# Kernel optimization log

Hardware: AMD Instinct MI355X
Metric: run time of the kernel (lower is better)

Reference implementation:

```python
import jax, jax.numpy as jnp
from jax import lax
import numpy as np

B = 16384
EPS = 1e-5


def conv2d(x, w, b, pad):
    # x: [N,C,H,W], w: [O,I,kh,kw]
    y = lax.conv_general_dilated(x, w, (1, 1), [(pad, pad), (pad, pad)],
                                 dimension_numbers=("NCHW", "OIHW", "NCHW"))
    return y + b[None, :, None, None]


def maxpool2(x):
    return lax.reduce_window(x, -jnp.inf, lax.max, (1, 1, 2, 2), (1, 1, 2, 2), "VALID")


def setup_inputs() -> dict:
    key = jax.random.key(0)
    ks = jax.random.split(key, 16)
    n = jax.random.normal
    return {
        "x": n(ks[0], (B, 1, 28, 28), dtype=jnp.float32),
        "conv1_w": n(ks[1], (8, 1, 3, 3), dtype=jnp.float32) * 0.2,
        "conv1_b": n(ks[2], (8,), dtype=jnp.float32) * 0.1,
        "conv2_w": n(ks[3], (16, 8, 3, 3), dtype=jnp.float32) * 0.1,
        "conv2_b": n(ks[4], (16,), dtype=jnp.float32) * 0.1,
        "s1_w": n(ks[5], (4, 2), dtype=jnp.float32) * 0.5,
        "s1_b": n(ks[6], (4,), dtype=jnp.float32) * 0.1,
        "s2_w": n(ks[7], (2, 4), dtype=jnp.float32) * 0.5,
        "s2_b": n(ks[8], (2,), dtype=jnp.float32) * 0.1,
        "filt_w": n(ks[9], (1, 1, 2, 2), dtype=jnp.float32) * 0.5,
        "filt_b": n(ks[10], (1,), dtype=jnp.float32) * 0.1,
        "fc1_w": n(ks[11], (64, 787), dtype=jnp.float32) * 0.03,
        "fc1_b": n(ks[12], (64,), dtype=jnp.float32) * 0.1,
        "fc2_w": n(ks[13], (4, 64), dtype=jnp.float32) * 0.1,
        "fc2_b": n(ks[14], (4,), dtype=jnp.float32) * 0.1,
        "bn_g": jnp.ones((4,), dtype=jnp.float32),
        "bn_b": jnp.zeros((4,), dtype=jnp.float32),
    }


def reference(x, conv1_w, conv1_b, conv2_w, conv2_b, s1_w, s1_b, s2_w, s2_b,
              filt_w, filt_b, fc1_w, fc1_b, fc2_w, fc2_b, bn_g, bn_b):
    bsz = x.shape[0]
    # feature extractor: conv3x3 -> relu -> maxpool2 (x2)
    f = maxpool2(jax.nn.relu(conv2d(x, conv1_w, conv1_b, 1)))        # [B,8,14,14]
    f = maxpool2(jax.nn.relu(conv2d(f, conv2_w, conv2_b, 1)))        # [B,16,7,7]
    flat = f.reshape(bsz, -1)                                        # [B,784]
    # sampler on first two features
    h = jnp.tanh(flat[:, :2] @ s1_w.T + s1_b)
    sampler_out = jax.nn.softmax(h @ s2_w.T + s2_b, axis=-1)         # [B,2]
    # conv filter: 2x2 stride-1 conv + sigmoid, mean over all patches
    logits = conv2d(x, filt_w, filt_b, 0)                            # [B,1,27,27]
    conv_out = jnp.mean(jax.nn.sigmoid(logits), axis=(1, 2, 3))[:, None]  # [B,1]
    combined = jnp.concatenate([flat, sampler_out, conv_out], axis=1)  # [B,787]
    out = jax.nn.relu(combined @ fc1_w.T + fc1_b) @ fc2_w.T + fc2_b    # [B,4]
    # BatchNorm1d, training mode (batch stats, biased variance)
    mu = jnp.mean(out, axis=0)
    var = jnp.var(out, axis=0)
    return (out - mu) * lax.rsqrt(var + EPS) * bn_g + bn_b
```

## Files before the change

kernel.cpp:

```cpp
#include <hip/hip_runtime.h>
#include <hip/hip_fp16.h>
#include <math.h>

#define NBATCH 16384
#define EPSV 1e-5f

typedef short short8 __attribute__((ext_vector_type(8)));
typedef _Float16 half8_t __attribute__((ext_vector_type(8)));
typedef short short2v __attribute__((ext_vector_type(2)));
typedef float f32x4 __attribute__((ext_vector_type(4)));
union V8 { uint4 u; short8 s; };
union VH { uint4 u; half8_t h; };

__device__ __forceinline__ unsigned short f2bf(float f) {
    unsigned int x = __float_as_uint(f);
    return (unsigned short)((x + 0x7fffu + ((x >> 16) & 1u)) >> 16);
}
__device__ __forceinline__ unsigned short f2h(float f) {
    return __half_as_ushort(__float2half(f));
}
__device__ __forceinline__ __half2 u2h(unsigned int u) { return __builtin_bit_cast(__half2, u); }
__device__ __forceinline__ unsigned int h2u(__half2 h) { return __builtin_bit_cast(unsigned int, h); }

__global__ __launch_bounds__(256) void k_prep(
    const float* __restrict__ fc1w, const float* __restrict__ w2,
    const float* __restrict__ w1, const float* __restrict__ b1,
    unsigned short* __restrict__ wt, unsigned short* __restrict__ af16,
    unsigned int* __restrict__ w1h2, unsigned int* __restrict__ b1h2)
{
    int i = blockIdx.x * 256 + threadIdx.x;
    if (i < 51200) {
        int n = i / 800, k = i - n * 800;
        float v = (k < 787) ? fc1w[n * 787 + k] : 0.f;
        wt[i] = f2h(v);
    } else if (i < 52736) {
        int a = i - 51200;
        int slot = a >> 7, rem = a & 127, oc = rem >> 3, ic = rem & 7;
        float v = (slot < 9) ? w2[oc * 72 + ic * 9 + slot] : 0.f;
        af16[a] = f2h(v);
    } else if (i < 52808) {
        int k = i - 52736;
        unsigned int hb = f2h(w1[k]);
        w1h2[k] = hb | (hb << 16);
    } else if (i < 52816) {
        int k = i - 52808;
        unsigned int hb = f2h(b1[k]);
        b1h2[k] = hb | (hb << 16);
    }
}

#define SXS 15

__global__ __launch_bounds__(64, 8) void k_conv(
    const float* __restrict__ x,
    const float* __restrict__ s1w, const float* __restrict__ s1b,
    const float* __restrict__ s2w, const float* __restrict__ s2b,
    const float* __restrict__ fw, const float* __restrict__ fb,
    const float* __restrict__ b2,
    const unsigned short* __restrict__ Afg,
    const unsigned int* __restrict__ w1h2g,
    const unsigned int* __restrict__ b1h2g,
    unsigned short* __restrict__ comb)
{
    const int l = threadIdx.x;

    __shared__ unsigned int sxu[30 * SXS];
    __shared__ __align__(16) unsigned short sf1[16 * 136];

    for (int i = l; i < 30 * SXS; i += 64) sxu[i] = 0u;
    if (l < 60) {
        int R, C;
        if (l < 16)      { R = 0;      C = l; }
        else if (l < 32) { R = 15;     C = l - 16; }
        else if (l < 46) { R = l - 31; C = 0; }
        else             { R = l - 45; C = 15; }
        *reinterpret_cast<uint4*>(&sf1[R * 136 + C * 8]) = uint4{0u, 0u, 0u, 0u};
    }

    const __half2 fwh0 = __float2half2_rn(fw[0]);
    const __half2 fwh1 = __float2half2_rn(fw[1]);
    const __half2 fwh2 = __float2half2_rn(fw[2]);
    const __half2 fwh3 = __float2half2_rn(fw[3]);
    const __half2 fbh  = __float2half2_rn(fb[0]);

    const int n = l & 15, g = l >> 4;
    const int qr = n & 7;
    const int q = (qr < 7) ? qr : 6;
    const int dr = n >> 3;
    int offs[3];
    VH af[3];
    #pragma unroll
    for (int s = 0; s < 3; ++s) {
        const int slot = s * 4 + g;
        const int u = slot / 3, v = slot - 3 * (slot / 3);
        offs[s] = (slot <= 8) ? (u * 136 + v * 8) : 0;
        af[s].u = *reinterpret_cast<const uint4*>(Afg + ((slot * 16 + n) << 3));
    }
    float biasv[4];
    #pragma unroll
    for (int i = 0; i < 4; ++i) biasv[i] = b2[4 * g + i];

    int srow[7], sww[7];
    #pragma unroll
    for (int k = 0; k < 7; ++k) {
        int u0 = l + k * 64;
        srow[k] = u0 / 15;
        sww[k]  = u0 - srow[k] * 15;
    }

    const int b = blockIdx.x;
    const float* xb = x + (size_t)b * 784;
    unsigned short* crow = comb + (size_t)b * 800;

    float xlo[7], xhi[7];
    #pragma unroll
    for (int k = 0; k < 7; ++k) {
        const int u0 = l + k * 64;
        if (u0 < 420) {
            const float* base = xb + srow[k] * 28;
            xlo[k] = (sww[k] == 0)  ? 0.f : base[2 * sww[k] - 1];
            xhi[k] = (sww[k] == 14) ? 0.f : base[2 * sww[k]];
        }
    }
    #pragma unroll
    for (int k = 0; k < 7; ++k) {
        const int u0 = l + k * 64;
        if (u0 < 420)
            sxu[(srow[k] + 1) * SXS + sww[k]] = h2u(__floats2half2_rn(xlo[k], xhi[k]));
    }

    float fsum = 0.f;
    for (int u0 = l; u0 < 378; u0 += 64) {
        int r = u0 / 14, cp = u0 - (u0 / 14) * 14;
        unsigned int A1 = sxu[(r + 1) * SXS + cp], B1 = sxu[(r + 1) * SXS + cp + 1];
        unsigned int A2 = sxu[(r + 2) * SXS + cp], B2 = sxu[(r + 2) * SXS + cp + 1];
        __half2 al1 = u2h(__builtin_amdgcn_alignbit(B1, A1, 16));
        __half2 al2 = u2h(__builtin_amdgcn_alignbit(B2, A2, 16));
        __half2 acc = __hfma2(fwh0, al1,
                      __hfma2(fwh1, u2h(B1),
                      __hfma2(fwh2, al2,
                      __hfma2(fwh3, u2h(B2), fbh))));
        float2 f = __half22float2(acc);
        fsum += __frcp_rn(1.f + __expf(-f.x));
        if (cp < 13) fsum += __frcp_rn(1.f + __expf(-f.y));
    }
    #pragma unroll
    for (int off = 32; off > 0; off >>= 1)
        fsum += __shfl_xor(fsum, off, 64);

    for (int i = l; i < 196; i += 64) {
        const int p = i / 14, j = i - (i / 14) * 14;
        unsigned int A[4], B[4], M[4];
        #pragma unroll
        for (int u = 0; u < 4; ++u) {
            A[u] = sxu[(2 * p + u) * SXS + j];
            B[u] = sxu[(2 * p + u) * SXS + j + 1];
            M[u] = __builtin_amdgcn_alignbit(B[u], A[u], 16);
        }
        unsigned short outv[8];
        #pragma unroll
        for (int oc = 0; oc < 8; ++oc) {
            __half2 a0 = u2h(b1h2g[oc]), a1 = a0;
            #pragma unroll
            for (int u = 0; u < 3; ++u) {
                #pragma unroll
                for (int v = 0; v < 3; ++v) {
                    const __half2 wv = u2h(w1h2g[oc * 9 + u * 3 + v]);
                    const unsigned int p0 = (v == 0) ? A[u]     : ((v == 1) ? M[u]     : B[u]);
                    const unsigned int p1 = (v == 0) ? A[u + 1] : ((v == 1) ? M[u + 1] : B[u + 1]);
                    a0 = __hfma2(wv, u2h(p0), a0);
                    a1 = __hfma2(wv, u2h(p1), a1);
                }
            }
            short2v s0 = __builtin_bit_cast(short2v, a0);
            short2v s1 = __builtin_bit_cast(short2v, a1);
            short2v mm = __builtin_elementwise_max(s0, s1);
            short m = mm[0] > mm[1] ? mm[0] : mm[1];
            if (m < 0) m = 0;
            outv[oc] = (unsigned short)m;
        }
        *reinterpret_cast<uint4*>(&sf1[(p + 1) * 136 + (j + 1) * 8]) =
            *reinterpret_cast<const uint4*>(outv);
    }

    float f0r = 0.f, f1r = 0.f;
    for (int pp = 0; pp < 7; ++pp) {
        const int rbase = (2 * pp + dr) * 136 + (2 * q) * 8;
        f32x4 acc0 = {0.f, 0.f, 0.f, 0.f}, acc1 = {0.f, 0.f, 0.f, 0.f};
        #pragma unroll
        for (int s = 0; s < 3; ++s) {
            VH b0, b1v;
            b0.u  = *reinterpret_cast<const uint4*>(&sf1[rbase + offs[s]]);
            b1v.u = *reinterpret_cast<const uint4*>(&sf1[rbase + 8 + offs[s]]);
            acc0 = __builtin_amdgcn_mfma_f32_16x16x32_f16(af[s].h, b0.h, acc0, 0, 0, 0);
            acc1 = __builtin_amdgcn_mfma_f32_16x16x32_f16(af[s].h, b1v.h, acc1, 0, 0, 0);
        }
        #pragma unroll
        for (int i = 0; i < 4; ++i) {
            float m = fmaxf(acc0[i], acc1[i]);
            m = fmaxf(m, __shfl_xor(m, 8, 64));
            float val = fmaxf(m + biasv[i], 0.f);
            if (pp == 0 && i == 0) {
                f0r = __shfl(val, 0, 64);
                f1r = __shfl(val, 1, 64);
            }
            if (n < 7)
                crow[(4 * g + i) * 49 + pp * 7 + q] = f2h(val);
        }
    }

    if (l < 13) crow[787 + l] = 0;
    if (l == 0) {
        crow[786] = f2h(fsum * (1.f / 729.f));
        float h[4];
        #pragma unroll
        for (int k = 0; k < 4; ++k) {
            float y = fmaf(f0r, s1w[2 * k], fmaf(f1r, s1w[2 * k + 1], s1b[k]));
            float e = __expf(2.f * y);
            h[k] = (e - 1.f) * __frcp_rn(e + 1.f);
        }
        float l0 = s2b[0], l1 = s2b[1];
        #pragma unroll
        for (int k = 0; k < 4; ++k) {
            l0 = fmaf(h[k], s2w[k], l0);
            l1 = fmaf(h[k], s2w[4 + k], l1);
        }
        float mx = fmaxf(l0, l1);
        float e0 = __expf(l0 - mx), e1 = __expf(l1 - mx);
        float inv = __frcp_rn(e0 + e1);
        crow[784] = f2h(e0 * inv);
        crow[785] = f2h(e1 * inv);
    }
}

__global__ __launch_bounds__(256) void k_fc(
    const unsigned short* __restrict__ A,
    const unsigned short* __restrict__ Bw,
    const float* __restrict__ fc1b,
    const float* __restrict__ fc2w, const float* __restrict__ fc2b,
    float* __restrict__ out, float* __restrict__ part)
{
    __shared__ uint4 Asm[2][256];
    __shared__ uint4 Bsm[2][256];
    __shared__ float sh[64][68];
    __shared__ float sfc2[4][64];
    __shared__ float pacc[4][8];

    const int t = threadIdx.x;
    const int w = t >> 6, l = t & 63;
    const int blk = blockIdx.x;

    sfc2[t >> 6][t & 63] = fc2w[t];

    const int srow = t >> 2, skbp = t & 3;
    const int skbl = skbp ^ ((srow >> 1) & 3);
    const uint4* Ag = reinterpret_cast<const uint4*>(A) + ((size_t)blk * 64 + srow) * 100;
    const uint4* Bg = reinterpret_cast<const uint4*>(Bw) + (size_t)srow * 100;
    const int sidx = srow * 4 + skbp;

    const int arow = w * 16 + (l & 15);
    const int aidx = arow * 4 + ((l >> 4) ^ ((arow >> 1) & 3));
    int bidx[4];
    #pragma unroll
    for (int nf = 0; nf < 4; ++nf) {
        int nn = nf * 16 + (l & 15);
        bidx[nf] = nn * 4 + ((l >> 4) ^ ((nn >> 1) & 3));
    }

    f32x4 acc0 = {0.f, 0.f, 0.f, 0.f}, acc1 = acc0, acc2 = acc0, acc3 = acc0;

    Asm[0][sidx] = Ag[skbl];
    Bsm[0][sidx] = Bg[skbl];

    int buf = 0;
    for (int s = 0; s < 25; ++s) {
        __syncthreads();
        if (s < 24) {
            Asm[buf ^ 1][sidx] = Ag[(s + 1) * 4 + skbl];
            Bsm[buf ^ 1][sidx] = Bg[(s + 1) * 4 + skbl];
        }
        VH av; av.u = Asm[buf][aidx];
        VH b0; b0.u = Bsm[buf][bidx[0]];
        VH b1; b1.u = Bsm[buf][bidx[1]];
        VH b2; b2.u = Bsm[buf][bidx[2]];
        VH b3; b3.u = Bsm[buf][bidx[3]];
        acc0 = __builtin_amdgcn_mfma_f32_16x16x32_f16(av.h, b0.h, acc0, 0, 0, 0);
        acc1 = __builtin_amdgcn_mfma_f32_16x16x32_f16(av.h, b1.h, acc1, 0, 0, 0);
        acc2 = __builtin_amdgcn_mfma_f32_16x16x32_f16(av.h, b2.h, acc2, 0, 0, 0);
        acc3 = __builtin_amdgcn_mfma_f32_16x16x32_f16(av.h, b3.h, acc3, 0, 0, 0);
        buf ^= 1;
    }

    {
        const int c0 = l & 15, r0 = w * 16 + (l >> 4) * 4;
        float fb0 = fc1b[c0], fb1 = fc1b[16 + c0], fb2 = fc1b[32 + c0], fb3 = fc1b[48 + c0];
        #pragma unroll
        for (int r = 0; r < 4; ++r) {
            sh[r0 + r][c0]      = fmaxf(acc0[r] + fb0, 0.f);
            sh[r0 + r][16 + c0] = fmaxf(acc1[r] + fb1, 0.f);
            sh[r0 + r][32 + c0] = fmaxf(acc2[r] + fb2, 0.f);
            sh[r0 + r][48 + c0] = fmaxf(acc3[r] + fb3, 0.f);
        }
    }
    __syncthreads();

    {
        const int row = t >> 2, oo = t & 3;
        float s = fc2b[oo];
        #pragma unroll 8
        for (int o = 0; o < 64; ++o)
            s = fmaf(sh[row][o], sfc2[oo][o], s);
        out[((size_t)blk * 64 + row) * 4 + oo] = s;

        float rs = s, rq = s * s;
        #pragma unroll
        for (int off = 4; off < 64; off <<= 1) {
            rs += __shfl_xor(rs, off, 64);
            rq += __shfl_xor(rq, off, 64);
        }
        if (l < 4) pacc[w][l] = rs;
        else if (l < 8) pacc[w][l] = rq;
    }
    __syncthreads();
    if (t < 8)
        part[blk * 8 + t] = pacc[0][t] + pacc[1][t] + pacc[2][t] + pacc[3][t];
}

__global__ void k_bnfinal(const float* __restrict__ part,
                          const float* __restrict__ g, const float* __restrict__ bb,
                          float* __restrict__ ss, int nblocks)
{
    const int t = threadIdx.x;
    float s[8];
    #pragma unroll
    for (int i = 0; i < 8; ++i) s[i] = 0.f;
    for (int idx = t; idx < nblocks; idx += 64)
        #pragma unroll
        for (int i = 0; i < 8; ++i) s[i] += part[idx * 8 + i];
    #pragma unroll
    for (int i = 0; i < 8; ++i)
        #pragma unroll
        for (int off = 32; off > 0; off >>= 1)
            s[i] += __shfl_xor(s[i], off, 64);
    if (t == 0) {
        const float invB = 1.f / 16384.f;
        #pragma unroll
        for (int j = 0; j < 4; ++j) {
            float mu = s[j] * invB;
            float var = s[4 + j] * invB - mu * mu;
            float sc = g[j] * rsqrtf(var + EPSV);
            ss[j] = sc;
            ss[4 + j] = bb[j] - mu * sc;
        }
    }
}

__global__ __launch_bounds__(256) void k_bnapply(const float* __restrict__ ss,
                                                 float* __restrict__ out)
{
    const int row = blockIdx.x * 256 + threadIdx.x;
    float4 v = reinterpret_cast<float4*>(out)[row];
    v.x = fmaf(v.x, ss[0], ss[4]);
    v.y = fmaf(v.y, ss[1], ss[5]);
    v.z = fmaf(v.z, ss[2], ss[6]);
    v.w = fmaf(v.w, ss[3], ss[7]);
    reinterpret_cast<float4*>(out)[row] = v;
}

__global__ __launch_bounds__(256) void k_transpose_fb(const float* __restrict__ in,
                                                      float* __restrict__ out)
{
    int i = blockIdx.x * 256 + threadIdx.x;
    if (i < 787 * 64) {
        int k = i >> 6, o = i & 63;
        out[i] = in[o * 787 + k];
    }
}

#define SF1F(ic, r, c) sf1[(ic) * 324 + (r) * 20 + (c)]

__global__ __launch_bounds__(256) void k_fused_fb(
    const float* __restrict__ x,
    const float* __restrict__ w1, const float* __restrict__ b1,
    const float* __restrict__ w2, const float* __restrict__ b2,
    const float* __restrict__ s1w, const float* __restrict__ s1b,
    const float* __restrict__ s2w, const float* __restrict__ s2b,
    const float* __restrict__ fw, const float* __restrict__ fb,
    const float* __restrict__ wt, const float* __restrict__ fc1b,
    const float* __restrict__ fc2w, const float* __restrict__ fc2b,
    float* __restrict__ pre)
{
    const int b = blockIdx.x;
    const int t = threadIdx.x;

    __shared__ float sxA[30][20];
    __shared__ float sxB[30][20];
    __shared__ float sf1[8 * 324];
    __shared__ float scomb[788];
    __shared__ float sw1[72];
    __shared__ float sb1[8];
    __shared__ float sw2p[16 * 76];
    __shared__ float sb2[16];
    __shared__ float sh1p[4][64];
    __shared__ float sh1[64];
    __shared__ float sred[4];
    __shared__ float ssm[27];

    for (int i = t; i < 600; i += 256) { (&sxA[0][0])[i] = 0.f; (&sxB[0][0])[i] = 0.f; }
    for (int i = t; i < 8 * 324; i += 256) sf1[i] = 0.f;
    if (t < 72) sw1[t] = w1[t];
    if (t < 8) sb1[t] = b1[t];
    for (int i = t; i < 1152; i += 256) {
        int oc = i / 72, rem = i - oc * 72;
        sw2p[oc * 76 + rem] = w2[i];
    }
    if (t < 16) sb2[t] = b2[t];
    if (t < 8) ssm[t] = s1w[t];
    else if (t < 12) ssm[t] = s1b[t - 8];
    else if (t < 20) ssm[t] = s2w[t - 12];
    else if (t < 22) ssm[t] = s2b[t - 20];
    else if (t < 26) ssm[t] = fw[t - 22];
    else if (t == 26) ssm[t] = fb[0];
    __syncthreads();

    const float* xb = x + (size_t)b * 784;
    for (int i = t; i < 784; i += 256) {
        int r = i / 28, c = i - (i / 28) * 28;
        float v = xb[i];
        int pr = r + 1, pc = c + 1;
        if (pc <= 15) sxA[pr][pc] = v;
        if (pc >= 14) sxB[pr][pc - 14] = v;
    }
    __syncthreads();

    {
        const float fw00 = ssm[22], fw01 = ssm[23], fw10 = ssm[24], fw11 = ssm[25];
        const float fbv = ssm[26];
        float fsum = 0.f;
        for (int i = t; i < 729; i += 256) {
            int r = i / 27, c = i - (i / 27) * 27;
            float x00, x01, x10, x11;
            if (c <= 13) {
                x00 = sxA[r + 1][c + 1]; x01 = sxA[r + 1][c + 2];
                x10 = sxA[r + 2][c + 1]; x11 = sxA[r + 2][c + 2];
            } else {
                int cb = c - 14;
                x00 = sxB[r + 1][cb + 1]; x01 = sxB[r + 1][cb + 2];
                x10 = sxB[r + 2][cb + 1]; x11 = sxB[r + 2][cb + 2];
            }
            float v = fbv;
            v = fmaf(x00, fw00, v); v = fmaf(x01, fw01, v);
            v = fmaf(x10, fw10, v); v = fmaf(x11, fw11, v);
            fsum += 1.f / (1.f + expf(-v));
        }
        #pragma unroll
        for (int off = 32; off > 0; off >>= 1)
            fsum += __shfl_xor(fsum, off, 64);
        if ((t & 63) == 0) sred[t >> 6] = fsum;
    }

    {
        const int half = t >> 7;
        const int id = t & 127;
        if (id < 112) {
            const int p = id >> 3, oc = id & 7;
            const float* base = half ? &sxB[0][0] : &sxA[0][0];
            float X[4][16];
            #pragma unroll
            for (int u = 0; u < 4; ++u) {
                const float4* rp = reinterpret_cast<const float4*>(base + (2 * p + u) * 20);
                float4 a = rp[0], bb4 = rp[1], c4 = rp[2], d4 = rp[3];
                X[u][0] = a.x;  X[u][1] = a.y;  X[u][2] = a.z;  X[u][3] = a.w;
                X[u][4] = bb4.x; X[u][5] = bb4.y; X[u][6] = bb4.z; X[u][7] = bb4.w;
                X[u][8] = c4.x;  X[u][9] = c4.y;  X[u][10] = c4.z; X[u][11] = c4.w;
                X[u][12] = d4.x; X[u][13] = d4.y; X[u][14] = d4.z; X[u][15] = d4.w;
            }
            float W[9];
            #pragma unroll
            for (int k = 0; k < 9; ++k) W[k] = sw1[oc * 9 + k];
            const float bias = sb1[oc];
            const int j0 = half * 7;
            #pragma unroll
            for (int jj = 0; jj < 7; ++jj) {
                float m = 0.f;
                #pragma unroll
                for (int dr = 0; dr < 2; ++dr)
                    #pragma unroll
                    for (int dc = 0; dc < 2; ++dc) {
                        float acc = bias;
                        #pragma unroll
                        for (int u = 0; u < 3; ++u)
                            #pragma unroll
                            for (int v = 0; v < 3; ++v)
                                acc = fmaf(X[dr + u][2 * jj + dc + v], W[u * 3 + v], acc);
                        m = fmaxf(m, acc);
                    }
                SF1F(oc, p + 1, j0 + jj + 1) = m;
            }
        }
    }
    __syncthreads();

    if (t < 112) {
        const int p = t >> 4, oc = t & 15;
        const float bias = sb2[oc];
        float acc[7][4];
        #pragma unroll
        for (int jj = 0; jj < 7; ++jj)
            #pragma unroll
            for (int s = 0; s < 4; ++s) acc[jj][s] = bias;
        for (int ic = 0; ic < 8; ++ic) {
            float X[4][16];
            #pragma unroll
            for (int u = 0; u < 4; ++u) {
                const float4* rp = reinterpret_cast<const float4*>(&SF1F(ic, 2 * p + u, 0));
                float4 a = rp[0], bb4 = rp[1], c4 = rp[2], d4 = rp[3];
                X[u][0] = a.x;  X[u][1] = a.y;  X[u][2] = a.z;  X[u][3] = a.w;
                X[u][4] = bb4.x; X[u][5] = bb4.y; X[u][6] = bb4.z; X[u][7] = bb4.w;
                X[u][8] = c4.x;  X[u][9] = c4.y;  X[u][10] = c4.z; X[u][11] = c4.w;
                X[u][12] = d4.x; X[u][13] = d4.y; X[u][14] = d4.z; X[u][15] = d4.w;
            }
            float W[9];
            #pragma unroll
            for (int k = 0; k < 9; ++k) W[k] = sw2p[oc * 76 + ic * 9 + k];
            #pragma unroll
            for (int jj = 0; jj < 7; ++jj)
                #pragma unroll
                for (int dr = 0; dr < 2; ++dr)
                    #pragma unroll
                    for (int dc = 0; dc < 2; ++dc)
                        #pragma unroll
                        for (int u = 0; u < 3; ++u)
                            #pragma unroll
                            for (int v = 0; v < 3; ++v)
                                acc[jj][dr * 2 + dc] =
                                    fmaf(X[dr + u][2 * jj + dc + v], W[u * 3 + v], acc[jj][dr * 2 + dc]);
        }
        #pragma unroll
        for (int jj = 0; jj < 7; ++jj) {
            float m = fmaxf(fmaxf(acc[jj][0], acc[jj][1]), fmaxf(acc[jj][2], acc[jj][3]));
            scomb[oc * 49 + p * 7 + jj] = fmaxf(m, 0.f);
        }
    }
    __syncthreads();

    if (t == 0) {
        scomb[786] = (sred[0] + sred[1] + sred[2] + sred[3]) * (1.f / 729.f);
        float f0 = scomb[0], f1 = scomb[1];
        float h[4];
        #pragma unroll
        for (int k = 0; k < 4; ++k)
            h[k] = tanhf(fmaf(f0, ssm[k * 2], fmaf(f1, ssm[k * 2 + 1], ssm[8 + k])));
        float l0 = ssm[20], l1 = ssm[21];
        #pragma unroll
        for (int k = 0; k < 4; ++k) {
            l0 = fmaf(h[k], ssm[12 + k], l0);
            l1 = fmaf(h[k], ssm[16 + k], l1);
        }
        float mx = fmaxf(l0, l1);
        float e0 = expf(l0 - mx), e1 = expf(l1 - mx);
        float inv = 1.f / (e0 + e1);
        scomb[784] = e0 * inv;
        scomb[785] = e1 * inv;
    }
    __syncthreads();

    {
        const int o = t & 63, w = t >> 6;
        const int k0 = w * 197;
        const int k1 = (w == 3) ? 787 : k0 + 197;
        const float* wp = wt + (size_t)k0 * 64 + o;
        float acc = 0.f;
        #pragma unroll 4
        for (int k = k0; k < k1; ++k) {
            acc = fmaf(scomb[k], *wp, acc);
            wp += 64;
        }
        sh1p[w][o] = acc;
    }
    __syncthreads();
    if (t < 64)
        sh1[t] = fmaxf(sh1p[0][t] + sh1p[1][t] + sh1p[2][t] + sh1p[3][t] + fc1b[t], 0.f);
    __syncthreads();

    {
        const int oo = t >> 6, lane = t & 63;
        float v = sh1[lane] * fc2w[oo * 64 + lane];
        #pragma unroll
        for (int off = 32; off > 0; off >>= 1)
            v += __shfl_xor(v, off, 64);
        if (lane == 0) pre[(size_t)b * 4 + oo] = v + fc2b[oo];
    }
}

__global__ __launch_bounds__(256) void k_bnstat_fb(const float* __restrict__ pre,
                                                   float* __restrict__ part)
{
    const int t = threadIdx.x;
    const int row = blockIdx.x * 256 + t;
    float4 v = reinterpret_cast<const float4*>(pre)[row];
    float s0 = v.x, s1 = v.y, s2 = v.z, s3 = v.w;
    float q0 = v.x * v.x, q1 = v.y * v.y, q2 = v.z * v.z, q3 = v.w * v.w;
    #pragma unroll
    for (int off = 32; off > 0; off >>= 1) {
        s0 += __shfl_xor(s0, off, 64);
        s1 += __shfl_xor(s1, off, 64);
        s2 += __shfl_xor(s2, off, 64);
        s3 += __shfl_xor(s3, off, 64);
        q0 += __shfl_xor(q0, off, 64);
        q1 += __shfl_xor(q1, off, 64);
        q2 += __shfl_xor(q2, off, 64);
        q3 += __shfl_xor(q3, off, 64);
    }
    __shared__ float acc[4][8];
    if ((t & 63) == 0) {
        int w = t >> 6;
        acc[w][0] = s0; acc[w][1] = s1; acc[w][2] = s2; acc[w][3] = s3;
        acc[w][4] = q0; acc[w][5] = q1; acc[w][6] = q2; acc[w][7] = q3;
    }
    __syncthreads();
    if (t < 8)
        part[blockIdx.x * 8 + t] = acc[0][t] + acc[1][t] + acc[2][t] + acc[3][t];
}

extern "C" void kernel_launch(void* const* d_in, const int* in_sizes, int n_in,
                              void* d_out, int out_size, void* d_ws, size_t ws_size,
                              hipStream_t stream)
{
    const float* x    = (const float*)d_in[0];
    const float* w1   = (const float*)d_in[1];
    const float* b1   = (const float*)d_in[2];
    const float* w2   = (const float*)d_in[3];
    const float* b2   = (const float*)d_in[4];
    const float* s1w  = (const float*)d_in[5];
    const float* s1b  = (const float*)d_in[6];
    const float* s2w  = (const float*)d_in[7];
    const float* s2b  = (const float*)d_in[8];
    const float* fw   = (const float*)d_in[9];
    const float* fb   = (const float*)d_in[10];
    const float* fc1w = (const float*)d_in[11];
    const float* fc1b = (const float*)d_in[12];
    const float* fc2w = (const float*)d_in[13];
    const float* fc2b = (const float*)d_in[14];
    const float* bng  = (const float*)d_in[15];
    const float* bnb  = (const float*)d_in[16];

    float* out = (float*)d_out;

    const size_t COMB_BYTES = (size_t)NBATCH * 800 * 2;
    const size_t WT_BYTES   = 64 * 800 * 2;
    const size_t AF16_BYTES = 1536 * 2;
    const size_t W1H2_BYTES = 72 * 4;
    const size_t B1H2_BYTES = 8 * 4;
    const size_t PART_BYTES = 256 * 8 * 4;
    const size_t NEED = COMB_BYTES + WT_BYTES + AF16_BYTES + W1H2_BYTES +
                        B1H2_BYTES + PART_BYTES + 32;

    if (ws_size >= NEED) {
        char* p = (char*)d_ws;
        unsigned short* comb = (unsigned short*)p;                     p += COMB_BYTES;
        unsigned short* wtbf = (unsigned short*)p;                     p += WT_BYTES;
        unsigned short* af16 = (unsigned short*)p;                     p += AF16_BYTES;
        unsigned int*   w1h2 = (unsigned int*)p;                       p += W1H2_BYTES;
        unsigned int*   b1h2 = (unsigned int*)p;                       p += B1H2_BYTES;
        float*          part = (float*)p;                              p += PART_BYTES;
        float*          ss   = (float*)p;

        k_prep<<<207, 256, 0, stream>>>(fc1w, w2, w1, b1, wtbf, af16, w1h2, b1h2);
        k_conv<<<NBATCH, 64, 0, stream>>>(x, s1w, s1b, s2w, s2b, fw, fb, b2,
                                          af16, w1h2, b1h2, comb);
        k_fc<<<256, 256, 0, stream>>>(comb, wtbf, fc1b, fc2w, fc2b, out, part);
        k_bnfinal<<<1, 64, 0, stream>>>(part, bng, bnb, ss, 256);
        k_bnapply<<<64, 256, 0, stream>>>(ss, out);
    } else {
        float* part = (float*)d_ws;
        float* ss   = part + 512;
        float* wt   = ss + 8;

        k_transpose_fb<<<197, 256, 0, stream>>>(fc1w, wt);
        k_fused_fb<<<NBATCH, 256, 0, stream>>>(x, w1, b1, w2, b2, s1w, s1b, s2w, s2b,
                                               fw, fb, wt, fc1b, fc2w, fc2b, out);
        k_bnstat_fb<<<64, 256, 0, stream>>>(out, part);
        k_bnfinal<<<1, 64, 0, stream>>>(part, bng, bnb, ss, 64);
        k_bnapply<<<64, 256, 0, stream>>>(ss, out);
    }
}
```

Baseline: 90.32 us.

## Store conv features position-major with packed writes, permute fc1 weights, batch LDS loads

The comb feature row is now written position-major (pos*16+oc), with four channels packed into an 8-byte store instead of four scattered 2-byte stores. The fc1 weight transpose in k_prep is permuted to match, so the matmul result is unchanged. The sigmoid-filter and conv1 loops are restructured to issue all LDS loads up front before computing, with a separate tail for the 4 leftover positions. The conv2 loop is fully unrolled with precomputed pointers, and the occupancy hint drops from 8 to 4 waves, trading occupancy for more registers.

```diff
diff --git a/kernel.cpp b/kernel.cpp
--- a/kernel.cpp
+++ b/kernel.cpp
@@ -31,7 +31,15 @@
     int i = blockIdx.x * 256 + threadIdx.x;
     if (i < 51200) {
         int n = i / 800, k = i - n * 800;
-        float v = (k < 787) ? fc1w[n * 787 + k] : 0.f;
+        float v;
+        if (k < 784) {
+            int pos = k >> 4, oc = k & 15;
+            v = fc1w[n * 787 + oc * 49 + pos];
+        } else if (k < 787) {
+            v = fc1w[n * 787 + k];
+        } else {
+            v = 0.f;
+        }
         wt[i] = f2h(v);
     } else if (i < 52736) {
         int a = i - 51200;
@@ -51,7 +59,7 @@
 
 #define SXS 15
 
-__global__ __launch_bounds__(64, 8) void k_conv(
+__global__ __launch_bounds__(64, 4) void k_conv(
     const float* __restrict__ x,
     const float* __restrict__ s1w, const float* __restrict__ s1b,
     const float* __restrict__ s2w, const float* __restrict__ s2b,
@@ -87,13 +95,14 @@
     const int qr = n & 7;
     const int q = (qr < 7) ? qr : 6;
     const int dr = n >> 3;
-    int offs[3];
     VH af[3];
+    const unsigned short* ps[3];
     #pragma unroll
     for (int s = 0; s < 3; ++s) {
         const int slot = s * 4 + g;
         const int u = slot / 3, v = slot - 3 * (slot / 3);
-        offs[s] = (slot <= 8) ? (u * 136 + v * 8) : 0;
+        const int offs = (slot <= 8) ? (u * 136 + v * 8) : 0;
+        ps[s] = sf1 + dr * 136 + 16 * q + offs;
         af[s].u = *reinterpret_cast<const uint4*>(Afg + ((slot * 16 + n) << 3));
     }
     float biasv[4];
@@ -111,6 +120,8 @@
     const int b = blockIdx.x;
     const float* xb = x + (size_t)b * 784;
     unsigned short* crow = comb + (size_t)b * 800;
+
+    if (l < 13) crow[787 + l] = 0;
 
     float xlo[7], xhi[7];
     #pragma unroll
@@ -130,86 +141,168 @@
     }
 
     float fsum = 0.f;
-    for (int u0 = l; u0 < 378; u0 += 64) {
-        int r = u0 / 14, cp = u0 - (u0 / 14) * 14;
-        unsigned int A1 = sxu[(r + 1) * SXS + cp], B1 = sxu[(r + 1) * SXS + cp + 1];
-        unsigned int A2 = sxu[(r + 2) * SXS + cp], B2 = sxu[(r + 2) * SXS + cp + 1];
-        __half2 al1 = u2h(__builtin_amdgcn_alignbit(B1, A1, 16));
-        __half2 al2 = u2h(__builtin_amdgcn_alignbit(B2, A2, 16));
-        __half2 acc = __hfma2(fwh0, al1,
-                      __hfma2(fwh1, u2h(B1),
-                      __hfma2(fwh2, al2,
-                      __hfma2(fwh3, u2h(B2), fbh))));
-        float2 f = __half22float2(acc);
-        fsum += __frcp_rn(1.f + __expf(-f.x));
-        if (cp < 13) fsum += __frcp_rn(1.f + __expf(-f.y));
-    }
-    #pragma unroll
-    for (int off = 32; off > 0; off >>= 1)
-        fsum += __shfl_xor(fsum, off, 64);
-
-    for (int i = l; i < 196; i += 64) {
-        const int p = i / 14, j = i - (i / 14) * 14;
-        unsigned int A[4], B[4], M[4];
-        #pragma unroll
-        for (int u = 0; u < 4; ++u) {
-            A[u] = sxu[(2 * p + u) * SXS + j];
-            B[u] = sxu[(2 * p + u) * SXS + j + 1];
-            M[u] = __builtin_amdgcn_alignbit(B[u], A[u], 16);
-        }
-        unsigned short outv[8];
-        #pragma unroll
-        for (int oc = 0; oc < 8; ++oc) {
-            __half2 a0 = u2h(b1h2g[oc]), a1 = a0;
-            #pragma unroll
-            for (int u = 0; u < 3; ++u) {
+    {
+        unsigned int FA1[6], FB1[6], FA2[6], FB2[6];
+        int fcp[6];
+        bool fv[6];
+        #pragma unroll
+        for (int k = 0; k < 6; ++k) {
+            int u0 = l + 64 * k;
+            fv[k] = (u0 < 378);
+            int uc = fv[k] ? u0 : 377;
+            int r = uc / 14, cp = uc - (uc / 14) * 14;
+            fcp[k] = cp;
+            FA1[k] = sxu[(r + 1) * SXS + cp]; FB1[k] = sxu[(r + 1) * SXS + cp + 1];
+            FA2[k] = sxu[(r + 2) * SXS + cp]; FB2[k] = sxu[(r + 2) * SXS + cp + 1];
+        }
+        #pragma unroll
+        for (int k = 0; k < 6; ++k) {
+            __half2 al1 = u2h(__builtin_amdgcn_alignbit(FB1[k], FA1[k], 16));
+            __half2 al2 = u2h(__builtin_amdgcn_alignbit(FB2[k], FA2[k], 16));
+            __half2 acc = __hfma2(fwh0, al1,
+                          __hfma2(fwh1, u2h(FB1[k]),
+                          __hfma2(fwh2, al2,
+                          __hfma2(fwh3, u2h(FB2[k]), fbh))));
+            float2 f = __half22float2(acc);
+            if (fv[k]) {
+                fsum += __frcp_rn(1.f + __expf(-f.x));
+                if (fcp[k] < 13) fsum += __frcp_rn(1.f + __expf(-f.y));
+            }
+        }
+        #pragma unroll
+        for (int off = 32; off > 0; off >>= 1)
+            fsum += __shfl_xor(fsum, off, 64);
+    }
+
+    {
+        unsigned int CA[3][4], CB[3][4];
+        int cpv[3], cjv[3];
+        #pragma unroll
+        for (int cc = 0; cc < 3; ++cc) {
+            const int i = l + cc * 64;
+            const int p = i / 14, j = i - (i / 14) * 14;
+            cpv[cc] = p; cjv[cc] = j;
+            #pragma unroll
+            for (int u = 0; u < 4; ++u) {
+                CA[cc][u] = sxu[(2 * p + u) * SXS + j];
+                CB[cc][u] = sxu[(2 * p + u) * SXS + j + 1];
+            }
+        }
+        #pragma unroll
+        for (int cc = 0; cc < 3; ++cc) {
+            unsigned int M[4];
+            #pragma unroll
+            for (int u = 0; u < 4; ++u)
+                M[u] = __builtin_amdgcn_alignbit(CB[cc][u], CA[cc][u], 16);
+            unsigned short outv[8];
+            #pragma unroll
+            for (int oc = 0; oc < 8; ++oc) {
+                __half2 a0 = u2h(b1h2g[oc]), a1 = a0;
                 #pragma unroll
-                for (int v = 0; v < 3; ++v) {
-                    const __half2 wv = u2h(w1h2g[oc * 9 + u * 3 + v]);
-                    const unsigned int p0 = (v == 0) ? A[u]     : ((v == 1) ? M[u]     : B[u]);
-                    const unsigned int p1 = (v == 0) ? A[u + 1] : ((v == 1) ? M[u + 1] : B[u + 1]);
-                    a0 = __hfma2(wv, u2h(p0), a0);
-                    a1 = __hfma2(wv, u2h(p1), a1);
+                for (int u = 0; u < 3; ++u) {
+                    #pragma unroll
+                    for (int v = 0; v < 3; ++v) {
+                        const __half2 wv = u2h(w1h2g[oc * 9 + u * 3 + v]);
+                        const unsigned int p0 = (v == 0) ? CA[cc][u]     : ((v == 1) ? M[u]     : CB[cc][u]);
+                        const unsigned int p1 = (v == 0) ? CA[cc][u + 1] : ((v == 1) ? M[u + 1] : CB[cc][u + 1]);
+                        a0 = __hfma2(wv, u2h(p0), a0);
+                        a1 = __hfma2(wv, u2h(p1), a1);
+                    }
                 }
-            }
-            short2v s0 = __builtin_bit_cast(short2v, a0);
-            short2v s1 = __builtin_bit_cast(short2v, a1);
-            short2v mm = __builtin_elementwise_max(s0, s1);
-            short m = mm[0] > mm[1] ? mm[0] : mm[1];
-            if (m < 0) m = 0;
-            outv[oc] = (unsigned short)m;
-        }
-        *reinterpret_cast<uint4*>(&sf1[(p + 1) * 136 + (j + 1) * 8]) =
-            *reinterpret_cast<const uint4*>(outv);
+                short2v s0 = __builtin_bit_cast(short2v, a0);
+                short2v s1 = __builtin_bit_cast(short2v, a1);
+                short2v mm = __builtin_elementwise_max(s0, s1);
+                short m = mm[0] > mm[1] ? mm[0] : mm[1];
+                if (m < 0) m = 0;
+                outv[oc] = (unsigned short)m;
+            }
+            *reinterpret_cast<uint4*>(&sf1[(cpv[cc] + 1) * 136 + (cjv[cc] + 1) * 8]) =
+                *reinterpret_cast<const uint4*>(outv);
+        }
+        if (l < 4) {
+            const int p = 13, j = 10 + l;
+            unsigned int A[4], B[4], M[4];
+            #pragma unroll
+            for (int u = 0; u < 4; ++u) {
+                A[u] = sxu[(2 * p + u) * SXS + j];
+                B[u] = sxu[(2 * p + u) * SXS + j + 1];
+                M[u] = __builtin_amdgcn_alignbit(B[u], A[u], 16);
+            }
+            unsigned short outv[8];
+            #pragma unroll
+            for (int oc = 0; oc < 8; ++oc) {
+                __half2 a0 = u2h(b1h2g[oc]), a1 = a0;
+                #pragma unroll
+                for (int u = 0; u < 3; ++u) {
+                    #pragma unroll
+                    for (int v = 0; v < 3; ++v) {
+                        const __half2 wv = u2h(w1h2g[oc * 9 + u * 3 + v]);
+                        const unsigned int p0 = (v == 0) ? A[u]     : ((v == 1) ? M[u]     : B[u]);
+                        const unsigned int p1 = (v == 0) ? A[u + 1] : ((v == 1) ? M[u + 1] : B[u + 1]);
+                        a0 = __hfma2(wv, u2h(p0), a0);
+                        a1 = __hfma2(wv, u2h(p1), a1);
+                    }
+                }
+                short2v s0 = __builtin_bit_cast(short2v, a0);
+                short2v s1 = __builtin_bit_cast(short2v, a1);
+                short2v mm = __builtin_elementwise_max(s0, s1);
+                short m = mm[0] > mm[1] ? mm[0] : mm[1];
+                if (m < 0) m = 0;
+                outv[oc] = (unsigned short)m;
+            }
+            *reinterpret_cast<uint4*>(&sf1[(p + 1) * 136 + (j + 1) * 8]) =
+                *reinterpret_cast<const uint4*>(outv);
+        }
     }
 
     float f0r = 0.f, f1r = 0.f;
+    #pragma unroll
     for (int pp = 0; pp < 7; ++pp) {
-        const int rbase = (2 * pp + dr) * 136 + (2 * q) * 8;
         f32x4 acc0 = {0.f, 0.f, 0.f, 0.f}, acc1 = {0.f, 0.f, 0.f, 0.f};
         #pragma unroll
         for (int s = 0; s < 3; ++s) {
             VH b0, b1v;
-            b0.u  = *reinterpret_cast<const uint4*>(&sf1[rbase + offs[s]]);
-            b1v.u = *reinterpret_cast<const uint4*>(&sf1[rbase + 8 + offs[s]]);
+            b0.u  = *reinterpret_cast<const uint4*>(ps[s] + pp * 272);
+            b1v.u = *reinterpret_cast<const uint4*>(ps[s] + pp * 272 + 8);
             acc0 = __builtin_amdgcn_mfma_f32_16x16x32_f16(af[s].h, b0.h, acc0, 0, 0, 0);
             acc1 = __builtin_amdgcn_mfma_f32_16x16x32_f16(af[s].h, b1v.h, acc1, 0, 0, 0);
         }
-        #pragma unroll
-        for (int i = 0; i < 4; ++i) {
-            float m = fmaxf(acc0[i], acc1[i]);
-            m = fmaxf(m, __shfl_xor(m, 8, 64));
-            float val = fmaxf(m + biasv[i], 0.f);
-            if (pp == 0 && i == 0) {
-                f0r = __shfl(val, 0, 64);
-                f1r = __shfl(val, 1, 64);
-            }
-            if (n < 7)
-                crow[(4 * g + i) * 49 + pp * 7 + q] = f2h(val);
-        }
-    }
-
-    if (l < 13) crow[787 + l] = 0;
+        unsigned int w0, w1p;
+        {
+            float v0, v1, v2, v3;
+            {
+                float m = fmaxf(acc0[0], acc1[0]);
+                m = fmaxf(m, __shfl_xor(m, 8, 64));
+                v0 = fmaxf(m + biasv[0], 0.f);
+            }
+            {
+                float m = fmaxf(acc0[1], acc1[1]);
+                m = fmaxf(m, __shfl_xor(m, 8, 64));
+                v1 = fmaxf(m + biasv[1], 0.f);
+            }
+            {
+                float m = fmaxf(acc0[2], acc1[2]);
+                m = fmaxf(m, __shfl_xor(m, 8, 64));
+                v2 = fmaxf(m + biasv[2], 0.f);
+            }
+            {
+                float m = fmaxf(acc0[3], acc1[3]);
+                m = fmaxf(m, __shfl_xor(m, 8, 64));
+                v3 = fmaxf(m + biasv[3], 0.f);
+            }
+            if (pp == 0) {
+                f0r = __shfl(v0, 0, 64);
+                f1r = __shfl(v0, 1, 64);
+            }
+            w0  = (unsigned int)f2h(v0) | ((unsigned int)f2h(v1) << 16);
+            w1p = (unsigned int)f2h(v2) | ((unsigned int)f2h(v3) << 16);
+        }
+        if (n < 7) {
+            uint2 pk = {w0, w1p};
+            *reinterpret_cast<uint2*>(&crow[(pp * 7 + q) * 16 + g * 4]) = pk;
+        }
+    }
+
     if (l == 0) {
         crow[786] = f2h(fsum * (1.f / 729.f));
         float h[4];
```

New measurement: 92.67 us. 1.03x slower.

## Process four images per conv block with prefetch and position-major feature layout

Applied to the files above, without the earlier changes.

Each conv workgroup now handles four images in sequence, loading the next image's input into registers while computing the current one. This amortizes per-block setup (weights, constants, shared-memory zeroing) and hides global-load latency. The combined feature row is stored position-major with packed 8-byte writes, and the fc1 weight prep permutes its columns to match. Fewer blocks and more registers (launch bounds lowered to 4 waves) reduce parallelism, and the shared buffers are reused across images without explicit barriers.

```diff
diff --git a/kernel.cpp b/kernel.cpp
--- a/kernel.cpp
+++ b/kernel.cpp
@@ -4,6 +4,7 @@
 
 #define NBATCH 16384
 #define EPSV 1e-5f
+#define IMGW 4
 
 typedef short short8 __attribute__((ext_vector_type(8)));
 typedef _Float16 half8_t __attribute__((ext_vector_type(8)));
@@ -31,7 +32,15 @@
     int i = blockIdx.x * 256 + threadIdx.x;
     if (i < 51200) {
         int n = i / 800, k = i - n * 800;
-        float v = (k < 787) ? fc1w[n * 787 + k] : 0.f;
+        float v;
+        if (k < 784) {
+            int pos = k >> 4, oc = k & 15;
+            v = fc1w[n * 787 + oc * 49 + pos];
+        } else if (k < 787) {
+            v = fc1w[n * 787 + k];
+        } else {
+            v = 0.f;
+        }
         wt[i] = f2h(v);
     } else if (i < 52736) {
         int a = i - 51200;
@@ -51,7 +60,7 @@
 
 #define SXS 15
 
-__global__ __launch_bounds__(64, 8) void k_conv(
+__global__ __launch_bounds__(64, 4) void k_conv(
     const float* __restrict__ x,
     const float* __restrict__ s1w, const float* __restrict__ s1b,
     const float* __restrict__ s2w, const float* __restrict__ s2b,
@@ -82,18 +91,27 @@
     const __half2 fwh2 = __float2half2_rn(fw[2]);
     const __half2 fwh3 = __float2half2_rn(fw[3]);
     const __half2 fbh  = __float2half2_rn(fb[0]);
+    float s1wv[8], s1bv[4], s2wv[8];
+    #pragma unroll
+    for (int k = 0; k < 8; ++k) s1wv[k] = s1w[k];
+    #pragma unroll
+    for (int k = 0; k < 4; ++k) s1bv[k] = s1b[k];
+    #pragma unroll
+    for (int k = 0; k < 8; ++k) s2wv[k] = s2w[k];
+    const float s2b0 = s2b[0], s2b1 = s2b[1];
 
     const int n = l & 15, g = l >> 4;
     const int qr = n & 7;
     const int q = (qr < 7) ? qr : 6;
     const int dr = n >> 3;
-    int offs[3];
     VH af[3];
+    const unsigned short* ps[3];
     #pragma unroll
     for (int s = 0; s < 3; ++s) {
         const int slot = s * 4 + g;
         const int u = slot / 3, v = slot - 3 * (slot / 3);
-        offs[s] = (slot <= 8) ? (u * 136 + v * 8) : 0;
+        const int offs = (slot <= 8) ? (u * 136 + v * 8) : 0;
+        ps[s] = sf1 + dr * 136 + 16 * q + offs;
         af[s].u = *reinterpret_cast<const uint4*>(Afg + ((slot * 16 + n) << 3));
     }
     float biasv[4];
@@ -108,128 +126,161 @@
         sww[k]  = u0 - srow[k] * 15;
     }
 
-    const int b = blockIdx.x;
-    const float* xb = x + (size_t)b * 784;
-    unsigned short* crow = comb + (size_t)b * 800;
+    const int b0 = blockIdx.x * IMGW;
 
     float xlo[7], xhi[7];
-    #pragma unroll
-    for (int k = 0; k < 7; ++k) {
-        const int u0 = l + k * 64;
-        if (u0 < 420) {
-            const float* base = xb + srow[k] * 28;
-            xlo[k] = (sww[k] == 0)  ? 0.f : base[2 * sww[k] - 1];
-            xhi[k] = (sww[k] == 14) ? 0.f : base[2 * sww[k]];
-        }
-    }
-    #pragma unroll
-    for (int k = 0; k < 7; ++k) {
-        const int u0 = l + k * 64;
-        if (u0 < 420)
-            sxu[(srow[k] + 1) * SXS + sww[k]] = h2u(__floats2half2_rn(xlo[k], xhi[k]));
-    }
-
-    float fsum = 0.f;
-    for (int u0 = l; u0 < 378; u0 += 64) {
-        int r = u0 / 14, cp = u0 - (u0 / 14) * 14;
-        unsigned int A1 = sxu[(r + 1) * SXS + cp], B1 = sxu[(r + 1) * SXS + cp + 1];
-        unsigned int A2 = sxu[(r + 2) * SXS + cp], B2 = sxu[(r + 2) * SXS + cp + 1];
-        __half2 al1 = u2h(__builtin_amdgcn_alignbit(B1, A1, 16));
-        __half2 al2 = u2h(__builtin_amdgcn_alignbit(B2, A2, 16));
-        __half2 acc = __hfma2(fwh0, al1,
-                      __hfma2(fwh1, u2h(B1),
-                      __hfma2(fwh2, al2,
-                      __hfma2(fwh3, u2h(B2), fbh))));
-        float2 f = __half22float2(acc);
-        fsum += __frcp_rn(1.f + __expf(-f.x));
-        if (cp < 13) fsum += __frcp_rn(1.f + __expf(-f.y));
-    }
-    #pragma unroll
-    for (int off = 32; off > 0; off >>= 1)
-        fsum += __shfl_xor(fsum, off, 64);
-
-    for (int i = l; i < 196; i += 64) {
-        const int p = i / 14, j = i - (i / 14) * 14;
-        unsigned int A[4], B[4], M[4];
-        #pragma unroll
-        for (int u = 0; u < 4; ++u) {
-            A[u] = sxu[(2 * p + u) * SXS + j];
-            B[u] = sxu[(2 * p + u) * SXS + j + 1];
-            M[u] = __builtin_amdgcn_alignbit(B[u], A[u], 16);
-        }
-        unsigned short outv[8];
-        #pragma unroll
-        for (int oc = 0; oc < 8; ++oc) {
-            __half2 a0 = u2h(b1h2g[oc]), a1 = a0;
-            #pragma unroll
-            for (int u = 0; u < 3; ++u) {
+    {
+        const float* xb = x + (size_t)b0 * 784;
+        #pragma unroll
+        for (int k = 0; k < 7; ++k) {
+            const int u0 = l + k * 64;
+            if (u0 < 420) {
+                const float* base = xb + srow[k] * 28;
+                xlo[k] = (sww[k] == 0)  ? 0.f : base[2 * sww[k] - 1];
+                xhi[k] = (sww[k] == 14) ? 0.f : base[2 * sww[k]];
+            }
+        }
+    }
+
+    #pragma unroll
+    for (int img = 0; img < IMGW; ++img) {
+        const int b = b0 + img;
+        unsigned short* crow = comb + (size_t)b * 800;
+
+        #pragma unroll
+        for (int k = 0; k < 7; ++k) {
+            const int u0 = l + k * 64;
+            if (u0 < 420)
+                sxu[(srow[k] + 1) * SXS + sww[k]] = h2u(__floats2half2_rn(xlo[k], xhi[k]));
+        }
+
+        float ylo[7], yhi[7];
+        if (img + 1 < IMGW) {
+            const float* xb = x + (size_t)(b + 1) * 784;
+            #pragma unroll
+            for (int k = 0; k < 7; ++k) {
+                const int u0 = l + k * 64;
+                if (u0 < 420) {
+                    const float* base = xb + srow[k] * 28;
+                    ylo[k] = (sww[k] == 0)  ? 0.f : base[2 * sww[k] - 1];
+                    yhi[k] = (sww[k] == 14) ? 0.f : base[2 * sww[k]];
+                }
+            }
+        }
+
+        if (l < 13) crow[787 + l] = 0;
+
+        float fsum = 0.f;
+        for (int u0 = l; u0 < 378; u0 += 64) {
+            int r = u0 / 14, cp = u0 - (u0 / 14) * 14;
+            unsigned int A1 = sxu[(r + 1) * SXS + cp], B1 = sxu[(r + 1) * SXS + cp + 1];
+            unsigned int A2 = sxu[(r + 2) * SXS + cp], B2 = sxu[(r + 2) * SXS + cp + 1];
+            __half2 al1 = u2h(__builtin_amdgcn_alignbit(B1, A1, 16));
+            __half2 al2 = u2h(__builtin_amdgcn_alignbit(B2, A2, 16));
+            __half2 acc = __hfma2(fwh0, al1,
+                          __hfma2(fwh1, u2h(B1),
+                          __hfma2(fwh2, al2,
+                          __hfma2(fwh3, u2h(B2), fbh))));
+            float2 f = __half22float2(acc);
+            fsum += __frcp_rn(1.f + __expf(-f.x));
+            if (cp < 13) fsum += __frcp_rn(1.f + __expf(-f.y));
+        }
+        #pragma unroll
+        for (int off = 32; off > 0; off >>= 1)
+            fsum += __shfl_xor(fsum, off, 64);
+
+        for (int i = l; i < 196; i += 64) {
+            const int p = i / 14, j = i - (i / 14) * 14;
+            unsigned int A[4], B[4], M[4];
+            #pragma unroll
+            for (int u = 0; u < 4; ++u) {
+                A[u] = sxu[(2 * p + u) * SXS + j];
+                B[u] = sxu[(2 * p + u) * SXS + j + 1];
+                M[u] = __builtin_amdgcn_alignbit(B[u], A[u], 16);
+            }
+            unsigned short outv[8];
+            #pragma unroll
+            for (int oc = 0; oc < 8; ++oc) {
+                __half2 a0 = u2h(b1h2g[oc]), a1 = a0;
                 #pragma unroll
-                for (int v = 0; v < 3; ++v) {
-                    const __half2 wv = u2h(w1h2g[oc * 9 + u * 3 + v]);
-                    const unsigned int p0 = (v == 0) ? A[u]     : ((v == 1) ? M[u]     : B[u]);
-                    const unsigned int p1 = (v == 0) ? A[u + 1] : ((v == 1) ? M[u + 1] : B[u + 1]);
-                    a0 = __hfma2(wv, u2h(p0), a0);
-                    a1 = __hfma2(wv, u2h(p1), a1);
+                for (int u = 0; u < 3; ++u) {
+                    #pragma unroll
+                    for (int v = 0; v < 3; ++v) {
+                        const __half2 wv = u2h(w1h2g[oc * 9 + u * 3 + v]);
+                        const unsigned int p0 = (v == 0) ? A[u]     : ((v == 1) ? M[u]     : B[u]);
+                        const unsigned int p1 = (v == 0) ? A[u + 1] : ((v == 1) ? M[u + 1] : B[u + 1]);
+                        a0 = __hfma2(wv, u2h(p0), a0);
+                        a1 = __hfma2(wv, u2h(p1), a1);
+                    }
                 }
-            }
-            short2v s0 = __builtin_bit_cast(short2v, a0);
-            short2v s1 = __builtin_bit_cast(short2v, a1);
-            short2v mm = __builtin_elementwise_max(s0, s1);
-            short m = mm[0] > mm[1] ? mm[0] : mm[1];
-            if (m < 0) m = 0;
-            outv[oc] = (unsigned short)m;
-        }
-        *reinterpret_cast<uint4*>(&sf1[(p + 1) * 136 + (j + 1) * 8]) =
-            *reinterpret_cast<const uint4*>(outv);
-    }
-
-    float f0r = 0.f, f1r = 0.f;
-    for (int pp = 0; pp < 7; ++pp) {
-        const int rbase = (2 * pp + dr) * 136 + (2 * q) * 8;
-        f32x4 acc0 = {0.f, 0.f, 0.f, 0.f}, acc1 = {0.f, 0.f, 0.f, 0.f};
-        #pragma unroll
-        for (int s = 0; s < 3; ++s) {
-            VH b0, b1v;
-            b0.u  = *reinterpret_cast<const uint4*>(&sf1[rbase + offs[s]]);
-            b1v.u = *reinterpret_cast<const uint4*>(&sf1[rbase + 8 + offs[s]]);
-            acc0 = __builtin_amdgcn_mfma_f32_16x16x32_f16(af[s].h, b0.h, acc0, 0, 0, 0);
-            acc1 = __builtin_amdgcn_mfma_f32_16x16x32_f16(af[s].h, b1v.h, acc1, 0, 0, 0);
-        }
-        #pragma unroll
-        for (int i = 0; i < 4; ++i) {
-            float m = fmaxf(acc0[i], acc1[i]);
-            m = fmaxf(m, __shfl_xor(m, 8, 64));
-            float val = fmaxf(m + biasv[i], 0.f);
-            if (pp == 0 && i == 0) {
-                f0r = __shfl(val, 0, 64);
-                f1r = __shfl(val, 1, 64);
-            }
-            if (n < 7)
-                crow[(4 * g + i) * 49 + pp * 7 + q] = f2h(val);
-        }
-    }
-
-    if (l < 13) crow[787 + l] = 0;
-    if (l == 0) {
-        crow[786] = f2h(fsum * (1.f / 729.f));
-        float h[4];
-        #pragma unroll
-        for (int k = 0; k < 4; ++k) {
-            float y = fmaf(f0r, s1w[2 * k], fmaf(f1r, s1w[2 * k + 1], s1b[k]));
-            float e = __expf(2.f * y);
-            h[k] = (e - 1.f) * __frcp_rn(e + 1.f);
-        }
-        float l0 = s2b[0], l1 = s2b[1];
-        #pragma unroll
-        for (int k = 0; k < 4; ++k) {
-            l0 = fmaf(h[k], s2w[k], l0);
-            l1 = fmaf(h[k], s2w[4 + k], l1);
-        }
-        float mx = fmaxf(l0, l1);
-        float e0 = __expf(l0 - mx), e1 = __expf(l1 - mx);
-        float inv = __frcp_rn(e0 + e1);
-        crow[784] = f2h(e0 * inv);
-        crow[785] = f2h(e1 * inv);
+                short2v s0 = __builtin_bit_cast(short2v, a0);
+                short2v s1 = __builtin_bit_cast(short2v, a1);
+                short2v mm = __builtin_elementwise_max(s0, s1);
+                short m = mm[0] > mm[1] ? mm[0] : mm[1];
+                if (m < 0) m = 0;
+                outv[oc] = (unsigned short)m;
+            }
+            *reinterpret_cast<uint4*>(&sf1[(p + 1) * 136 + (j + 1) * 8]) =
+                *reinterpret_cast<const uint4*>(outv);
+        }
+
+        float f0r = 0.f, f1r = 0.f;
+        #pragma unroll
+        for (int pp = 0; pp < 7; ++pp) {
+            f32x4 acc0 = {0.f, 0.f, 0.f, 0.f}, acc1 = {0.f, 0.f, 0.f, 0.f};
+            #pragma unroll
+            for (int s = 0; s < 3; ++s) {
+                VH c0, c1;
+                c0.u = *reinterpret_cast<const uint4*>(ps[s] + pp * 272);
+                c1.u = *reinterpret_cast<const uint4*>(ps[s] + pp * 272 + 8);
+                acc0 = __builtin_amdgcn_mfma_f32_16x16x32_f16(af[s].h, c0.h, acc0, 0, 0, 0);
+                acc1 = __builtin_amdgcn_mfma_f32_16x16x32_f16(af[s].h, c1.h, acc1, 0, 0, 0);
+            }
+            float vv[4];
+            #pragma unroll
+            for (int i = 0; i < 4; ++i) {
+                float m = fmaxf(acc0[i], acc1[i]);
+                m = fmaxf(m, __shfl_xor(m, 8, 64));
+                vv[i] = fmaxf(m + biasv[i], 0.f);
+            }
+            if (pp == 0) {
+                f0r = __shfl(vv[0], 0, 64);
+                f1r = __shfl(vv[0], 1, 64);
+            }
+            if (n < 7) {
+                uint2 pk;
+                pk.x = (unsigned int)f2h(vv[0]) | ((unsigned int)f2h(vv[1]) << 16);
+                pk.y = (unsigned int)f2h(vv[2]) | ((unsigned int)f2h(vv[3]) << 16);
+                *reinterpret_cast<uint2*>(&crow[(pp * 7 + q) * 16 + g * 4]) = pk;
+            }
+        }
+
+        if (l == 0) {
+            crow[786] = f2h(fsum * (1.f / 729.f));
+            float h[4];
+            #pragma unroll
+            for (int k = 0; k < 4; ++k) {
+                float y = fmaf(f0r, s1wv[2 * k], fmaf(f1r, s1wv[2 * k + 1], s1bv[k]));
+                float e = __expf(2.f * y);
+                h[k] = (e - 1.f) * __frcp_rn(e + 1.f);
+            }
+            float l0 = s2b0, l1 = s2b1;
+            #pragma unroll
+            for (int k = 0; k < 4; ++k) {
+                l0 = fmaf(h[k], s2wv[k], l0);
+                l1 = fmaf(h[k], s2wv[4 + k], l1);
+            }
+            float mx = fmaxf(l0, l1);
+            float e0 = __expf(l0 - mx), e1 = __expf(l1 - mx);
+            float inv = __frcp_rn(e0 + e1);
+            crow[784] = f2h(e0 * inv);
+            crow[785] = f2h(e1 * inv);
+        }
+
+        if (img + 1 < IMGW) {
+            #pragma unroll
+            for (int k = 0; k < 7; ++k) { xlo[k] = ylo[k]; xhi[k] = yhi[k]; }
+        }
     }
 }
 
@@ -667,8 +718,8 @@
         float*          ss   = (float*)p;
 
         k_prep<<<207, 256, 0, stream>>>(fc1w, w2, w1, b1, wtbf, af16, w1h2, b1h2);
-        k_conv<<<NBATCH, 64, 0, stream>>>(x, s1w, s1b, s2w, s2b, fw, fb, b2,
-                                          af16, w1h2, b1h2, comb);
+        k_conv<<<NBATCH / IMGW, 64, 0, stream>>>(x, s1w, s1b, s2w, s2b, fw, fb, b2,
+                                                 af16, w1h2, b1h2, comb);
         k_fc<<<256, 256, 0, stream>>>(comb, wtbf, fc1b, fc2w, fc2b, out, part);
         k_bnfinal<<<1, 64, 0, stream>>>(part, bng, bnb, ss, 256);
         k_bnapply<<<64, 256, 0, stream>>>(ss, out);
```

Result: slower. 95.64 us (+5.9%).
